# Performance work log

Measured on AMD Instinct MI355X. Metric: run time of the kernel, lower is better.

The kernel has to match this reference:

```python
import jax, jax.numpy as jnp
import numpy as np

N_NODES = 50000


def gcn_conv(x, src, dst, norm, W, b, n):
    # PyG GCNConv: out = A_hat @ (x W) + b, with A_hat = D^-1/2 (A+I) D^-1/2
    h = x @ W                                   # [N, out]
    msgs = norm[:, None] * h[src]               # [E+N, out]
    out = jax.ops.segment_sum(msgs, dst, num_segments=n)
    return out + b


def _norm_and_loops(edge_index, n):
    # add self loops
    loops = jnp.arange(n, dtype=edge_index.dtype)
    src = jnp.concatenate([edge_index[0], loops])
    dst = jnp.concatenate([edge_index[1], loops])
    ones = jnp.ones(src.shape[0], dtype=jnp.float32)
    deg = jax.ops.segment_sum(ones, dst, num_segments=n)
    dinv = jnp.where(deg > 0, jax.lax.rsqrt(jnp.maximum(deg, 1e-12)), 0.0)
    norm = dinv[src] * dinv[dst]
    return src, dst, norm


def setup_inputs() -> dict:
    key = jax.random.key(0)
    k1, k2, k3, k4, k5, k6 = jax.random.split(key, 6)
    F_in, H, C = 1433, 128, 7
    x = jax.random.normal(k1, (N_NODES, F_in), dtype=jnp.float32)
    edge_index = jax.random.randint(k2, (2, 1600000), 0, N_NODES, dtype=jnp.int64)
    W1 = jax.random.normal(k3, (F_in, H), dtype=jnp.float32) / np.sqrt(F_in)
    b1 = jnp.zeros((H,), dtype=jnp.float32)
    W2 = jax.random.normal(k4, (H, C), dtype=jnp.float32) / np.sqrt(H)
    b2 = jnp.zeros((C,), dtype=jnp.float32)
    return {"x": x, "edge_index": edge_index, "W1": W1, "b1": b1, "W2": W2, "b2": b2}


def reference(x, edge_index, W1, b1, W2, b2):
    n = x.shape[0]
    src, dst, norm = _norm_and_loops(edge_index, n)
    h = gcn_conv(x, src, dst, norm, W1, b1, n)
    h = jax.nn.relu(h)
    # dropout p=0.5 is identity in eval mode
    out = gcn_conv(h, src, dst, norm, W2, b2, n)
    return out
```

## Files before the change

### kernel.cpp

```cpp
#include <hip/hip_runtime.h>
#include <hip/hip_bf16.h>

typedef __attribute__((ext_vector_type(8))) short short8_t;
typedef __attribute__((ext_vector_type(4))) float f32x4;
typedef float f32x4u __attribute__((ext_vector_type(4), aligned(4)));

#define NNODES 50000
#define FIN 1433
#define HID 128
#define NCLS 7
#define KT1 45
#define BK 32
#define BM 128
#define CAP 96
#define GSTR 1040

static __device__ __forceinline__ unsigned short f2bf(float f) {
    union { float f; unsigned int u; } v; v.f = f;
    unsigned int u = v.u;
    u += 0x7FFFu + ((u >> 16) & 1u);
    return (unsigned short)(u >> 16);
}
static __device__ __forceinline__ float u2f(unsigned int u) {
    union { unsigned int u; float f; } v; v.u = u; return v.f;
}

__global__ void prep_w1(const float* __restrict__ W1, unsigned short* __restrict__ W1s) {
    int tid = blockIdx.x * 512 + threadIdx.x;
    if (tid >= KT1 * 512) return;
    int kt = tid >> 9, seg = tid & 511;
    int c = seg & 127, g = seg >> 7;
    int kb = kt * BK + g * 8;
    unsigned int w[4];
    #pragma unroll
    for (int p = 0; p < 4; ++p) {
        int k0 = kb + p * 2, k1 = kb + p * 2 + 1;
        unsigned short lo = (k0 < FIN) ? f2bf(W1[(size_t)k0 * HID + c]) : (unsigned short)0;
        unsigned short hi = (k1 < FIN) ? f2bf(W1[(size_t)k1 * HID + c]) : (unsigned short)0;
        w[p] = (unsigned int)lo | ((unsigned int)hi << 16);
    }
    uint4* dstp = (uint4*)(W1s + (size_t)tid * 8);
    uint4 val; val.x = w[0]; val.y = w[1]; val.z = w[2]; val.w = w[3];
    *dstp = val;
}

__global__ __launch_bounds__(512) void gemm_fill(const float* __restrict__ x,
                                                 const unsigned short* __restrict__ W1s,
                                                 unsigned short* __restrict__ h, int M,
                                                 const int* __restrict__ src,
                                                 const int* __restrict__ dst, int E,
                                                 int* __restrict__ cnt,
                                                 int* __restrict__ csr_f,
                                                 int* __restrict__ ovf_cnt,
                                                 int2* __restrict__ ovf, int gb) {
    __shared__ unsigned short As[2][4160];
    __shared__ unsigned short Bs[3][4096];

    if (blockIdx.x >= gb) {
        int bid = blockIdx.x - gb;
        int i = (bid * 512 + (int)threadIdx.x) * 8;
        int lim = min(i + 8, E);
        for (int e = i; e < lim; ++e) {
            int d = dst[e], s = src[e];
            int pos = atomicAdd(&cnt[d], 1);
            if (pos < CAP) csr_f[d * CAP + pos] = s;
            else { int op = atomicAdd(ovf_cnt, 1); ovf[op] = make_int2(d, s); }
        }
        return;
    }

    const int t = threadIdx.x;
    const int wave = t >> 6, lane = t & 63;
    const int wm = wave >> 1, wn = wave & 1;
    const int r = lane & 15, u = lane >> 4;
    const int rowBase = blockIdx.x * BM;
    f32x4 acc[2][4] = {};

    float4 areg[2];

    auto issueA = [&](int kt) {
        int k0 = kt * BK;
        #pragma unroll
        for (int i = 0; i < 2; ++i) {
            int quad = i * 512 + t;
            int row = quad >> 3, kq = quad & 7;
            int gr = min(rowBase + row, M - 1);
            int gk = k0 + kq * 4;
            f32x4u v = *(const f32x4u*)(x + (size_t)gr * FIN + gk);
            areg[i].x = v.x; areg[i].y = v.y; areg[i].z = v.z; areg[i].w = v.w;
        }
    };
    auto issueA_tail = [&]() {
        #pragma unroll
        for (int i = 0; i < 2; ++i) {
            int quad = i * 512 + t;
            int row = quad >> 3, kq = quad & 7;
            int gr = min(rowBase + row, M - 1);
            int gk = 1408 + kq * 4;
            const float* p = x + (size_t)gr * FIN;
            areg[i].x = (gk + 0 < FIN) ? p[gk + 0] : 0.f;
            areg[i].y = (gk + 1 < FIN) ? p[gk + 1] : 0.f;
            areg[i].z = (gk + 2 < FIN) ? p[gk + 2] : 0.f;
            areg[i].w = (gk + 3 < FIN) ? p[gk + 3] : 0.f;
        }
    };
    auto issueB = [&](int kt, int buf) {
        const unsigned short* gp = W1s + ((size_t)kt * 512 + t) * 8;
        unsigned short* lp = &Bs[buf][(wave * 64) * 8];
        __builtin_amdgcn_global_load_lds(
            (const __attribute__((address_space(1))) unsigned int*)gp,
            (__attribute__((address_space(3))) unsigned int*)lp, 16, 0, 0);
    };
    auto writeA = [&](int buf) {
        #pragma unroll
        for (int i = 0; i < 2; ++i) {
            int quad = i * 512 + t;
            int row = quad >> 3, kq = quad & 7;
            __hip_bfloat162 lo2 = __float22bfloat162_rn(make_float2(areg[i].x, areg[i].y));
            __hip_bfloat162 hi2 = __float22bfloat162_rn(make_float2(areg[i].z, areg[i].w));
            unsigned int ulo, uhi;
            __builtin_memcpy(&ulo, &lo2, 4);
            __builtin_memcpy(&uhi, &hi2, 4);
            unsigned long long pk = ((unsigned long long)uhi << 32) | (unsigned long long)ulo;
            int g = kq >> 1, half = kq & 1;
            int us = ((g ^ (row & 3)) * GSTR) + row * 8 + half * 4;
            *(unsigned long long*)(&As[buf][us]) = pk;
        }
    };
    auto compute = [&](int kt) {
        const int abuf = kt & 1, bbuf = kt % 3;
        short8_t af[2], bfr[4];
        #pragma unroll
        for (int mi = 0; mi < 2; ++mi) {
            int row = wm * 32 + mi * 16 + r;
            int us = ((u ^ (row & 3)) * GSTR) + row * 8;
            af[mi] = *(const short8_t*)(&As[abuf][us]);
        }
        #pragma unroll
        for (int ni = 0; ni < 4; ++ni) {
            int c = wn * 64 + ni * 16 + r;
            bfr[ni] = *(const short8_t*)(&Bs[bbuf][u * 1024 + c * 8]);
        }
        #pragma unroll
        for (int mi = 0; mi < 2; ++mi)
            #pragma unroll
            for (int ni = 0; ni < 4; ++ni)
                acc[mi][ni] = __builtin_amdgcn_mfma_f32_16x16x32_bf16(af[mi], bfr[ni], acc[mi][ni], 0, 0, 0);
    };

    issueA(0); issueB(0, 0);
    writeA(0);
    issueA(1); issueB(1, 1);
    __syncthreads();

    for (int kt = 0; kt < KT1 - 3; ++kt) {
        compute(kt);
        writeA((kt + 1) & 1);
        issueA(kt + 2);
        issueB(kt + 2, (kt + 2) % 3);
        __syncthreads();
    }
    {
        compute(KT1 - 3);
        writeA((KT1 - 2) & 1);
        __syncthreads();
    }
    issueA_tail();
    issueB(KT1 - 1, (KT1 - 1) % 3);
    writeA((KT1 - 1) & 1);
    __syncthreads();
    compute(KT1 - 2);
    compute(KT1 - 1);

    #pragma unroll
    for (int mi = 0; mi < 2; ++mi) {
        #pragma unroll
        for (int reg = 0; reg < 4; ++reg) {
            int grow = rowBase + wm * 32 + mi * 16 + u * 4 + reg;
            if (grow < M) {
                #pragma unroll
                for (int ni = 0; ni < 4; ++ni) {
                    int gcol = wn * 64 + ni * 16 + r;
                    h[(size_t)grow * HID + gcol] = f2bf(acc[mi][ni][reg]);
                }
            }
        }
    }
}

__global__ void self_dinv(int* __restrict__ cnt, int* __restrict__ csr_f,
                          float* __restrict__ dinv,
                          int* __restrict__ ovf_cnt, int2* __restrict__ ovf, int n) {
    int i = blockIdx.x * 256 + threadIdx.x;
    if (i >= n) return;
    int c = cnt[i];
    if (c < CAP) csr_f[i * CAP + c] = i;
    else { int op = atomicAdd(ovf_cnt, 1); ovf[op] = make_int2(i, i); }
    cnt[i] = c + 1;
    dinv[i] = rsqrtf((float)(c + 1));
}

__global__ __launch_bounds__(256) void agg1(const unsigned short* __restrict__ h,
                                            const int* __restrict__ cnt,
                                            const int* __restrict__ csr_f,
                                            const float* __restrict__ dinv,
                                            const float* __restrict__ b1,
                                            const float* __restrict__ W2,
                                            const int* __restrict__ ovf_cnt,
                                            const int2* __restrict__ ovf,
                                            float* __restrict__ h2s, int n) {
    __shared__ float W2s[HID * NCLS];
    for (int i = threadIdx.x; i < HID * NCLS; i += 256) W2s[i] = W2[i];
    __syncthreads();
    int wave = threadIdx.x >> 6, lane = threadIdx.x & 63;
    int v = blockIdx.x * 4 + wave;
    if (v >= n) return;
    const int fr = lane & 15, g = lane >> 4;
    int total = cnt[v];
    int inrow = min(total, CAP);
    const int base = v * CAP;
    float acc[8] = {};
    #pragma unroll 4
    for (int j = g; j < inrow; j += 4) {
        int s = csr_f[base + j];
        float ds = dinv[s];
        uint4 q = *(const uint4*)(h + (size_t)s * HID + fr * 8);
        unsigned int w[4] = {q.x, q.y, q.z, q.w};
        #pragma unroll
        for (int p = 0; p < 4; ++p) {
            acc[p * 2 + 0] += ds * u2f(w[p] << 16);
            acc[p * 2 + 1] += ds * u2f(w[p] & 0xffff0000u);
        }
    }
    if (__builtin_expect(total > CAP, 0) && g == 0) {
        int on = *ovf_cnt;
        for (int k = 0; k < on; ++k) {
            int2 pr = ovf[k];
            if (pr.x == v) {
                int s = pr.y;
                float ds = dinv[s];
                uint4 q = *(const uint4*)(h + (size_t)s * HID + fr * 8);
                unsigned int w[4] = {q.x, q.y, q.z, q.w};
                #pragma unroll
                for (int p = 0; p < 4; ++p) {
                    acc[p * 2 + 0] += ds * u2f(w[p] << 16);
                    acc[p * 2 + 1] += ds * u2f(w[p] & 0xffff0000u);
                }
            }
        }
    }
    #pragma unroll
    for (int e = 0; e < 8; ++e) {
        acc[e] += __shfl_xor(acc[e], 16, 64);
        acc[e] += __shfl_xor(acc[e], 32, 64);
    }
    float dv = dinv[v];
    float p[NCLS];
    #pragma unroll
    for (int c = 0; c < NCLS; ++c) p[c] = 0.f;
    #pragma unroll
    for (int e = 0; e < 8; ++e) {
        int f = fr * 8 + e;
        float val = fmaxf(dv * acc[e] + b1[f], 0.f);
        #pragma unroll
        for (int c = 0; c < NCLS; ++c) p[c] += val * W2s[f * NCLS + c];
    }
    #pragma unroll
    for (int off = 8; off >= 1; off >>= 1)
        #pragma unroll
        for (int c = 0; c < NCLS; ++c)
            p[c] += __shfl_xor(p[c], off, 64);
    if (lane == 0) {
        #pragma unroll
        for (int c = 0; c < NCLS; ++c) h2s[(size_t)v * 8 + c] = dv * p[c];
        h2s[(size_t)v * 8 + 7] = 0.f;
    }
}

__global__ __launch_bounds__(256) void agg2(const float* __restrict__ h2s,
                                            const int* __restrict__ cnt,
                                            const int* __restrict__ csr_f,
                                            const float* __restrict__ dinv,
                                            const float* __restrict__ b2,
                                            const int* __restrict__ ovf_cnt,
                                            const int2* __restrict__ ovf,
                                            float* __restrict__ out, int n) {
    int wave = threadIdx.x >> 6, lane = threadIdx.x & 63;
    int half = lane >> 5;
    int c = lane & 7, g = (lane >> 3) & 3;
    int v = blockIdx.x * 8 + wave * 2 + half;
    if (v >= n) return;
    int total = cnt[v];
    int inrow = min(total, CAP);
    const int base = v * CAP;
    float acc = 0.f;
    #pragma unroll 4
    for (int j = g; j < inrow; j += 4) {
        int s = csr_f[base + j];
        acc += h2s[(size_t)s * 8 + c];
    }
    if (__builtin_expect(total > CAP, 0) && g == 0) {
        int on = *ovf_cnt;
        for (int k = 0; k < on; ++k) {
            int2 pr = ovf[k];
            if (pr.x == v) acc += h2s[(size_t)pr.y * 8 + c];
        }
    }
    acc += __shfl_xor(acc, 8, 64);
    acc += __shfl_xor(acc, 16, 64);
    if (g == 0 && c < NCLS) out[(size_t)v * NCLS + c] = dinv[v] * acc + b2[c];
}

extern "C" void kernel_launch(void* const* d_in, const int* in_sizes, int n_in,
                              void* d_out, int out_size, void* d_ws, size_t ws_size,
                              hipStream_t stream) {
    const float* x  = (const float*)d_in[0];
    const int*   ei = (const int*)d_in[1];
    const float* W1 = (const float*)d_in[2];
    const float* b1 = (const float*)d_in[3];
    const float* W2 = (const float*)d_in[4];
    const float* b2 = (const float*)d_in[5];
    float* out = (float*)d_out;

    const int N = NNODES;
    const int E = in_sizes[1] / 2;
    const int* src = ei;
    const int* dst = ei + E;
    const int GB = (N + BM - 1) / BM;
    const int FB = (E + 4095) / 4096;

    char* ws = (char*)d_ws;
    size_t off = 0;
    auto alloc = [&](size_t bytes) {
        void* p = ws + off;
        off += (bytes + 255) & ~(size_t)255;
        return p;
    };
    int*   cnt     = (int*)alloc((size_t)N * 4);
    int*   ovf_cnt = (int*)alloc(4);
    float* dinv    = (float*)alloc((size_t)N * 4);
    int*   csr_f   = (int*)alloc((size_t)N * CAP * 4);
    int2*  ovf     = (int2*)alloc((size_t)4096 * 8);
    unsigned short* W1s = (unsigned short*)alloc((size_t)KT1 * 512 * 8 * 2);
    unsigned short* h   = (unsigned short*)alloc((size_t)N * HID * 2);
    float* h2s     = (float*)alloc((size_t)N * 8 * 4);

    hipMemsetAsync(cnt, 0, ((char*)ovf_cnt - (char*)cnt) + 256, stream);
    prep_w1<<<(KT1 * 512 + 511) / 512, 512, 0, stream>>>(W1, W1s);
    gemm_fill<<<GB + FB, 512, 0, stream>>>(x, W1s, h, N, src, dst, E,
                                           cnt, csr_f, ovf_cnt, ovf, GB);
    self_dinv<<<(N + 255) / 256, 256, 0, stream>>>(cnt, csr_f, dinv, ovf_cnt, ovf, N);
    agg1<<<(N + 3) / 4, 256, 0, stream>>>(h, cnt, csr_f, dinv, b1, W2, ovf_cnt, ovf, h2s, N);
    agg2<<<(N + 7) / 8, 256, 0, stream>>>(h2s, cnt, csr_f, dinv, b2, ovf_cnt, ovf, out, N);
}
```

Measured before the change: 238.5 us.

## Restructure GEMM to stage full 32-row A panel in LDS, stream W1 from global

The pipelined 128-row tiled GEMM with LDS double/triple buffering is replaced by a 32-row block that loads its entire bf16 A panel (all of K) into LDS once, then has each of 16 waves compute one 16x16 output tile by reading B fragments straight from global memory. Block size goes to 1024 threads and the fused edge-fill blocks are resized to match. The aim is to drop per-k-step barriers and pipeline bookkeeping and to raise the number of blocks. In exchange, W1 reuse per block falls sharply, so each block rereads B from global/L2, and the large LDS footprint (about 92KB) limits occupancy with no overlap between loading and compute.

Measured after the change: 279.1 us. 1.17x slower.

```diff
diff --git a/kernel.cpp b/kernel.cpp
--- a/kernel.cpp
+++ b/kernel.cpp
@@ -11,9 +11,9 @@
 #define NCLS 7
 #define KT1 45
 #define BK 32
-#define BM 128
+#define BM 32
+#define ROWSTR 1448
 #define CAP 96
-#define GSTR 1040
 
 static __device__ __forceinline__ unsigned short f2bf(float f) {
     union { float f; unsigned int u; } v; v.f = f;
@@ -44,21 +44,20 @@
     *dstp = val;
 }
 
-__global__ __launch_bounds__(512) void gemm_fill(const float* __restrict__ x,
-                                                 const unsigned short* __restrict__ W1s,
-                                                 unsigned short* __restrict__ h, int M,
-                                                 const int* __restrict__ src,
-                                                 const int* __restrict__ dst, int E,
-                                                 int* __restrict__ cnt,
-                                                 int* __restrict__ csr_f,
-                                                 int* __restrict__ ovf_cnt,
-                                                 int2* __restrict__ ovf, int gb) {
-    __shared__ unsigned short As[2][4160];
-    __shared__ unsigned short Bs[3][4096];
+__global__ __launch_bounds__(1024) void gemm_fill(const float* __restrict__ x,
+                                                  const unsigned short* __restrict__ W1s,
+                                                  unsigned short* __restrict__ h, int M,
+                                                  const int* __restrict__ src,
+                                                  const int* __restrict__ dst, int E,
+                                                  int* __restrict__ cnt,
+                                                  int* __restrict__ csr_f,
+                                                  int* __restrict__ ovf_cnt,
+                                                  int2* __restrict__ ovf, int gb) {
+    __shared__ unsigned short As[BM * ROWSTR];
 
     if (blockIdx.x >= gb) {
         int bid = blockIdx.x - gb;
-        int i = (bid * 512 + (int)threadIdx.x) * 8;
+        int i = (bid * 1024 + (int)threadIdx.x) * 8;
         int lim = min(i + 8, E);
         for (int e = i; e < lim; ++e) {
             int d = dst[e], s = src[e];
@@ -70,120 +69,52 @@
     }
 
     const int t = threadIdx.x;
+    const int rowBase = blockIdx.x * BM;
+
+    for (int j = t; j < BM * 360; j += 1024) {
+        int row = j / 360, q = j - row * 360;
+        int k = q * 4;
+        int gr = min(rowBase + row, M - 1);
+        float4 v;
+        if (k + 3 < FIN) {
+            f32x4u vv = *(const f32x4u*)(x + (size_t)gr * FIN + k);
+            v.x = vv.x; v.y = vv.y; v.z = vv.z; v.w = vv.w;
+        } else {
+            const float* p = x + (size_t)gr * FIN;
+            v.x = (k + 0 < FIN) ? p[k + 0] : 0.f;
+            v.y = (k + 1 < FIN) ? p[k + 1] : 0.f;
+            v.z = (k + 2 < FIN) ? p[k + 2] : 0.f;
+            v.w = (k + 3 < FIN) ? p[k + 3] : 0.f;
+        }
+        __hip_bfloat162 lo2 = __float22bfloat162_rn(make_float2(v.x, v.y));
+        __hip_bfloat162 hi2 = __float22bfloat162_rn(make_float2(v.z, v.w));
+        unsigned int ulo, uhi;
+        __builtin_memcpy(&ulo, &lo2, 4);
+        __builtin_memcpy(&uhi, &hi2, 4);
+        unsigned long long pk = ((unsigned long long)uhi << 32) | (unsigned long long)ulo;
+        *(unsigned long long*)(&As[row * ROWSTR + k]) = pk;
+    }
+    __syncthreads();
+
     const int wave = t >> 6, lane = t & 63;
-    const int wm = wave >> 1, wn = wave & 1;
+    const int rowt = wave & 1, colt = wave >> 1;
     const int r = lane & 15, u = lane >> 4;
-    const int rowBase = blockIdx.x * BM;
-    f32x4 acc[2][4] = {};
-
-    float4 areg[2];
-
-    auto issueA = [&](int kt) {
-        int k0 = kt * BK;
-        #pragma unroll
-        for (int i = 0; i < 2; ++i) {
-            int quad = i * 512 + t;
-            int row = quad >> 3, kq = quad & 7;
-            int gr = min(rowBase + row, M - 1);
-            int gk = k0 + kq * 4;
-            f32x4u v = *(const f32x4u*)(x + (size_t)gr * FIN + gk);
-            areg[i].x = v.x; areg[i].y = v.y; areg[i].z = v.z; areg[i].w = v.w;
-        }
-    };
-    auto issueA_tail = [&]() {
-        #pragma unroll
-        for (int i = 0; i < 2; ++i) {
-            int quad = i * 512 + t;
-            int row = quad >> 3, kq = quad & 7;
-            int gr = min(rowBase + row, M - 1);
-            int gk = 1408 + kq * 4;
-            const float* p = x + (size_t)gr * FIN;
-            areg[i].x = (gk + 0 < FIN) ? p[gk + 0] : 0.f;
-            areg[i].y = (gk + 1 < FIN) ? p[gk + 1] : 0.f;
-            areg[i].z = (gk + 2 < FIN) ? p[gk + 2] : 0.f;
-            areg[i].w = (gk + 3 < FIN) ? p[gk + 3] : 0.f;
-        }
-    };
-    auto issueB = [&](int kt, int buf) {
-        const unsigned short* gp = W1s + ((size_t)kt * 512 + t) * 8;
-        unsigned short* lp = &Bs[buf][(wave * 64) * 8];
-        __builtin_amdgcn_global_load_lds(
-            (const __attribute__((address_space(1))) unsigned int*)gp,
-            (__attribute__((address_space(3))) unsigned int*)lp, 16, 0, 0);
-    };
-    auto writeA = [&](int buf) {
-        #pragma unroll
-        for (int i = 0; i < 2; ++i) {
-            int quad = i * 512 + t;
-            int row = quad >> 3, kq = quad & 7;
-            __hip_bfloat162 lo2 = __float22bfloat162_rn(make_float2(areg[i].x, areg[i].y));
-            __hip_bfloat162 hi2 = __float22bfloat162_rn(make_float2(areg[i].z, areg[i].w));
-            unsigned int ulo, uhi;
-            __builtin_memcpy(&ulo, &lo2, 4);
-            __builtin_memcpy(&uhi, &hi2, 4);
-            unsigned long long pk = ((unsigned long long)uhi << 32) | (unsigned long long)ulo;
-            int g = kq >> 1, half = kq & 1;
-            int us = ((g ^ (row & 3)) * GSTR) + row * 8 + half * 4;
-            *(unsigned long long*)(&As[buf][us]) = pk;
-        }
-    };
-    auto compute = [&](int kt) {
-        const int abuf = kt & 1, bbuf = kt % 3;
-        short8_t af[2], bfr[4];
-        #pragma unroll
-        for (int mi = 0; mi < 2; ++mi) {
-            int row = wm * 32 + mi * 16 + r;
-            int us = ((u ^ (row & 3)) * GSTR) + row * 8;
-            af[mi] = *(const short8_t*)(&As[abuf][us]);
-        }
-        #pragma unroll
-        for (int ni = 0; ni < 4; ++ni) {
-            int c = wn * 64 + ni * 16 + r;
-            bfr[ni] = *(const short8_t*)(&Bs[bbuf][u * 1024 + c * 8]);
-        }
-        #pragma unroll
-        for (int mi = 0; mi < 2; ++mi)
-            #pragma unroll
-            for (int ni = 0; ni < 4; ++ni)
-                acc[mi][ni] = __builtin_amdgcn_mfma_f32_16x16x32_bf16(af[mi], bfr[ni], acc[mi][ni], 0, 0, 0);
-    };
-
-    issueA(0); issueB(0, 0);
-    writeA(0);
-    issueA(1); issueB(1, 1);
-    __syncthreads();
-
-    for (int kt = 0; kt < KT1 - 3; ++kt) {
-        compute(kt);
-        writeA((kt + 1) & 1);
-        issueA(kt + 2);
-        issueB(kt + 2, (kt + 2) % 3);
-        __syncthreads();
-    }
-    {
-        compute(KT1 - 3);
-        writeA((KT1 - 2) & 1);
-        __syncthreads();
-    }
-    issueA_tail();
-    issueB(KT1 - 1, (KT1 - 1) % 3);
-    writeA((KT1 - 1) & 1);
-    __syncthreads();
-    compute(KT1 - 2);
-    compute(KT1 - 1);
-
-    #pragma unroll
-    for (int mi = 0; mi < 2; ++mi) {
-        #pragma unroll
-        for (int reg = 0; reg < 4; ++reg) {
-            int grow = rowBase + wm * 32 + mi * 16 + u * 4 + reg;
-            if (grow < M) {
-                #pragma unroll
-                for (int ni = 0; ni < 4; ++ni) {
-                    int gcol = wn * 64 + ni * 16 + r;
-                    h[(size_t)grow * HID + gcol] = f2bf(acc[mi][ni][reg]);
-                }
-            }
+    const unsigned short* As_base = As + (rowt * 16 + r) * ROWSTR + u * 8;
+    const unsigned short* bp = W1s + ((size_t)(u * 128 + colt * 16 + r)) * 8;
+    f32x4 acc = {};
+    #pragma unroll 5
+    for (int kt = 0; kt < KT1; ++kt) {
+        short8_t a = *(const short8_t*)(As_base + kt * 32);
+        short8_t b = *(const short8_t*)(bp + (size_t)kt * 4096);
+        acc = __builtin_amdgcn_mfma_f32_16x16x32_bf16(a, b, acc, 0, 0, 0);
+    }
+
+    #pragma unroll
+    for (int reg = 0; reg < 4; ++reg) {
+        int grow = rowBase + rowt * 16 + u * 4 + reg;
+        if (grow < M) {
+            int gcol = colt * 16 + r;
+            h[(size_t)grow * HID + gcol] = f2bf(acc[reg]);
         }
     }
 }
@@ -327,7 +258,7 @@
     const int* src = ei;
     const int* dst = ei + E;
     const int GB = (N + BM - 1) / BM;
-    const int FB = (E + 4095) / 4096;
+    const int FB = (E + 8191) / 8192;
 
     char* ws = (char*)d_ws;
     size_t off = 0;
@@ -347,8 +278,8 @@
 
     hipMemsetAsync(cnt, 0, ((char*)ovf_cnt - (char*)cnt) + 256, stream);
     prep_w1<<<(KT1 * 512 + 511) / 512, 512, 0, stream>>>(W1, W1s);
-    gemm_fill<<<GB + FB, 512, 0, stream>>>(x, W1s, h, N, src, dst, E,
-                                           cnt, csr_f, ovf_cnt, ovf, GB);
+    gemm_fill<<<GB + FB, 1024, 0, stream>>>(x, W1s, h, N, src, dst, E,
+                                            cnt, csr_f, ovf_cnt, ovf, GB);
     self_dinv<<<(N + 255) / 256, 256, 0, stream>>>(cnt, csr_f, dinv, ovf_cnt, ovf, N);
     agg1<<<(N + 3) / 4, 256, 0, stream>>>(h, cnt, csr_f, dinv, b1, W2, ovf_cnt, ovf, h2s, N);
     agg2<<<(N + 7) / 8, 256, 0, stream>>>(h2s, cnt, csr_f, dinv, b2, ovf_cnt, ovf, out, N);
```
